# Optimization experiments

Hardware: AMD Instinct MI355X
Metric: run time of the kernel (lower is better)

The kernel has to match this reference:

```python
import jax, jax.numpy as jnp
import numpy as np

T, D, H, HD = 4096, 1536, 12, 128  # tokens, hidden, heads, head_dim
NEG = -1e9


def rotate_half(x):
    x1, x2 = jnp.split(x, 2, axis=-1)
    return jnp.concatenate((-x2, x1), axis=-1)


def setup_inputs() -> dict:
    key = jax.random.key(0)
    k1, k2, k3, k4 = jax.random.split(key, 4)
    hidden_states = jax.random.normal(k1, (T, D), dtype=jnp.float32)
    cu_seqlens = (jnp.arange(5, dtype=jnp.int32) * (T // 4))  # [0,1024,2048,3072,4096]
    # rotary angles: positions within each segment times inverse frequencies
    pos = jnp.arange(T, dtype=jnp.float32) % (T // 4)
    inv_freq = 1.0 / (10000.0 ** (jnp.arange(0, HD // 2, dtype=jnp.float32) / (HD // 2)))
    rotary_pos_emb = pos[:, None] * inv_freq[None, :]  # (T, HD//2)
    w_qkv = jax.random.normal(k2, (3 * D, D), dtype=jnp.float32) * (D ** -0.5)
    w_proj = jax.random.normal(k3, (D, D), dtype=jnp.float32) * (D ** -0.5)
    return {"hidden_states": hidden_states, "cu_seqlens": cu_seqlens,
            "rotary_pos_emb": rotary_pos_emb, "w_qkv": w_qkv, "w_proj": w_proj}


def reference(hidden_states, cu_seqlens, rotary_pos_emb, w_qkv, w_proj):
    seq_len = hidden_states.shape[0]
    scaling = HD ** -0.5
    # fused QKV projection: (T, 3D) -> (3, T, H, HD)
    qkv = (hidden_states @ w_qkv.T).reshape(seq_len, 3, H, HD).transpose(1, 0, 2, 3)
    q, k, v = qkv[0], qkv[1], qkv[2]
    # RoPE (vision style): emb = cat(rpe, rpe) along last dim
    emb = jnp.concatenate((rotary_pos_emb, rotary_pos_emb), axis=-1)  # (T, HD)
    cos = jnp.cos(emb)[:, None, :]  # (T, 1, HD) broadcast over heads
    sin = jnp.sin(emb)[:, None, :]
    q = q * cos + rotate_half(q) * sin
    k = k * cos + rotate_half(k) * sin
    # block-diagonal mask from cu_seqlens (varlen packing)
    seg_id = jnp.searchsorted(cu_seqlens[1:], jnp.arange(seq_len), side="right")
    block_mask = seg_id[:, None] == seg_id[None, :]  # (T, T) bool
    # attention per head: (H, T, HD)
    qh = q.transpose(1, 0, 2)
    kh = k.transpose(1, 0, 2)
    vh = v.transpose(1, 0, 2)
    scores = jnp.einsum("htd,hsd->hts", qh, kh) * scaling
    scores = jnp.where(block_mask[None, :, :], scores, NEG)
    attn = jax.nn.softmax(scores, axis=-1)
    out = jnp.einsum("hts,hsd->htd", attn, vh)  # (H, T, HD)
    out = out.transpose(1, 0, 2).reshape(seq_len, D)
    return out @ w_proj.T


if __name__ == "__main__":
    o = reference(**setup_inputs())
    print(o.shape, o.dtype)
```

## Files before the change

kernel.cpp:

```cpp
#include <hip/hip_runtime.h>
#include <stdint.h>

#define TT 4096
#define DD 1536
#define NH 12
#define HD_ 128

typedef __bf16 bf16x8 __attribute__((ext_vector_type(8)));
typedef float  f32x4  __attribute__((ext_vector_type(4)));
typedef float  f32x16 __attribute__((ext_vector_type(16)));

__device__ __forceinline__ unsigned short f2b(float f) {
  union { float f; uint32_t u; } x; x.f = f;
  uint32_t r = x.u + 0x7fffu + ((x.u >> 16) & 1u);
  return (unsigned short)(r >> 16);
}
__device__ __forceinline__ float b2f(unsigned short b) {
  union { uint32_t u; float f; } x; x.u = ((uint32_t)b) << 16;
  return x.f;
}

__device__ __forceinline__ f32x16 mfma32(bf16x8 a, bf16x8 b, f32x16 c) {
  return __builtin_amdgcn_mfma_f32_32x32x16_bf16(a, b, c, 0, 0, 0);
}

__device__ __forceinline__ void async16(const void* g, void* l) {
  __builtin_amdgcn_global_load_lds((const __attribute__((address_space(1))) uint32_t*)g,
                                   (__attribute__((address_space(3))) uint32_t*)l,
                                   16, 0, 0);
}

__global__ void aux_kernel(const float* __restrict__ hs,
                           const float* __restrict__ wqkv,
                           const float* __restrict__ rpe,
                           unsigned short* __restrict__ hb,
                           unsigned short* __restrict__ wq,
                           float* __restrict__ cs, float* __restrict__ sn) {
  const int b = blockIdx.x;
  if (b < 13056) {
    const float* in = (b < 6144) ? hs : wqkv;
    unsigned short* out = (b < 6144) ? hb : wq;
    const int base = (b < 6144) ? b : (b - 6144);
    int i = (base * 256 + threadIdx.x) * 4;
    float4 v = *reinterpret_cast<const float4*>(in + i);
    ushort4 o;
    o.x = f2b(v.x); o.y = f2b(v.y); o.z = f2b(v.z); o.w = f2b(v.w);
    *reinterpret_cast<ushort4*>(out + i) = o;
  } else {
    int i = (b - 13056) * 256 + threadIdx.x;
    float e = rpe[i];
    float s, c;
    sincosf(e, &s, &c);
    cs[i] = c;
    sn[i] = s;
  }
}

__global__ void cast_bf16_kernel(const float* __restrict__ in,
                                 unsigned short* __restrict__ out, int n) {
  int i = (blockIdx.x * blockDim.x + threadIdx.x) * 4;
  if (i + 3 < n) {
    float4 v = *reinterpret_cast<const float4*>(in + i);
    ushort4 o;
    o.x = f2b(v.x); o.y = f2b(v.y); o.z = f2b(v.z); o.w = f2b(v.w);
    *reinterpret_cast<ushort4*>(out + i) = o;
  }
}

__global__ __launch_bounds__(256, 4) void gemm_qkv_kernel(
    const unsigned short* __restrict__ A, const unsigned short* __restrict__ B,
    unsigned short* __restrict__ Qp, unsigned short* __restrict__ Kp,
    unsigned short* __restrict__ Vt, const float* __restrict__ csT,
    const float* __restrict__ snT) {
  __shared__ char smem[32768];
  const int tid = threadIdx.x;
  const int lane = tid & 63;
  const int wave = tid >> 6;
  const int wm = wave >> 1, wn = wave & 1;
  const int lr = lane & 15, lh = lane >> 4;

  const int m0 = blockIdx.x * 128;
  const int n0 = blockIdx.y * 128;

  const int srow = tid >> 2;
  const int schunk = (tid & 3) ^ (srow & 3);
  const unsigned short* Ag = A + (size_t)(m0 + srow) * DD + schunk * 8;
  const unsigned short* Bg = B + (size_t)(n0 + srow) * DD + schunk * 8;

#define STAGE_G(BUF, K0)                                            \
  {                                                                 \
    unsigned short* la = (unsigned short*)(smem + (BUF) * 16384);   \
    unsigned short* lb = la + 4096;                                 \
    async16(Ag + (K0), &la[tid * 8]);                               \
    async16(Ag + (K0) + (size_t)64 * DD, &la[2048 + tid * 8]);      \
    async16(Bg + (K0), &lb[tid * 8]);                               \
    async16(Bg + (K0) + (size_t)64 * DD, &lb[2048 + tid * 8]);      \
  }

  const int csw = (lr & 3);
  f32x4 acc[4][4] = {};
  STAGE_G(0, 0);
  __syncthreads();
  int cur = 0;
  for (int k0 = 0; k0 < DD; k0 += 32) {
    const int kn = (k0 + 32 < DD) ? (k0 + 32) : k0;
    STAGE_G(cur ^ 1, kn);
    const unsigned short* la = (const unsigned short*)(smem + cur * 16384);
    const unsigned short* lb = la + 4096;
    bf16x8 af[4], bfr[4];
#pragma unroll
    for (int i = 0; i < 4; i++) {
      af[i]  = *reinterpret_cast<const bf16x8*>(
          &la[(wm * 64 + i * 16 + lr) * 32 + (lh ^ csw) * 8]);
      bfr[i] = *reinterpret_cast<const bf16x8*>(
          &lb[(i * 32 + wn * 16 + lr) * 32 + (lh ^ csw) * 8]);
    }
#pragma unroll
    for (int i = 0; i < 4; i++)
#pragma unroll
      for (int j = 0; j < 4; j++)
        acc[i][j] = __builtin_amdgcn_mfma_f32_16x16x32_bf16(af[i], bfr[j], acc[i][j], 0, 0, 0);
    __syncthreads();
    cur ^= 1;
  }
#undef STAGE_G

  const int s  = n0 / DD;
  const int hh = (n0 - s * DD) >> 7;

  if (s == 2) {
#pragma unroll
    for (int i = 0; i < 4; i++)
#pragma unroll
      for (int j = 0; j < 4; j++) {
        const int dd = j * 32 + wn * 16 + lr;
        const int t0 = m0 + wm * 64 + i * 16 + lh * 4;
        ushort4 st;
        st.x = f2b(acc[i][j][0]); st.y = f2b(acc[i][j][1]);
        st.z = f2b(acc[i][j][2]); st.w = f2b(acc[i][j][3]);
        *reinterpret_cast<ushort4*>(&Vt[((size_t)(hh * HD_ + dd)) * TT + t0]) = st;
      }
  } else {
    unsigned short* dst = (s == 0) ? Qp : Kp;
    const float scale =
        (s == 0) ? (0.08838834764831845f * 1.4426950408889634f) : 1.0f;
#pragma unroll
    for (int i = 0; i < 4; i++) {
#pragma unroll
      for (int j = 0; j < 4; j++) {
        const int dd = j * 32 + wn * 16 + lr;
        const int d2 = dd & 63;
        const float sgn = (dd < 64) ? -1.f : 1.f;
#pragma unroll
        for (int r = 0; r < 4; r++) {
          const int t = m0 + wm * 64 + i * 16 + lh * 4 + r;
          const float own = acc[i][j][r];
          const float par = acc[i][j ^ 2][r];
          const float c   = csT[t * 64 + d2];
          const float sn_ = snT[t * 64 + d2];
          dst[((size_t)hh * TT + t) * HD_ + dd] =
              f2b((own * c + sgn * par * sn_) * scale);
        }
        __builtin_amdgcn_sched_barrier(0);
      }
    }
  }
}

__global__ __launch_bounds__(512) void attn_kernel(
    const unsigned short* __restrict__ Qp, const unsigned short* __restrict__ Kp,
    const unsigned short* __restrict__ Vt, const int* __restrict__ cu,
    unsigned short* __restrict__ AO) {
  __shared__ unsigned short lds[32768];
  const int bid = blockIdx.x;
  const int tid = threadIdx.x;
  const int wave = tid >> 6;
  const int lane = tid & 63;
  const int lq = lane & 31;
  const int hi = lane >> 5;
  const int swz = lq & 7;

  const int xcd  = bid & 7;
  const int idx  = bid >> 3;
  const int pair = xcd * 6 + (idx >> 2);
  const int qblk = idx & 3;
  const int h    = pair >> 2;
  const int seg  = pair & 3;
  const int kstart = cu[seg], kend = cu[seg + 1];
  const int q0 = kstart + (qblk * 8 + wave) * 32;

  const unsigned short* Kh = Kp + (size_t)h * TT * HD_;
  const unsigned short* Vh = Vt + (size_t)h * HD_ * TT;

  const int krow0 = tid >> 4, kc0 = tid & 15;
  const int vrow0 = tid >> 3, vc0 = tid & 7;

#define STAGE_TILE(BUF, KT)                                                    \
  {                                                                            \
    unsigned short* Lk = &lds[(BUF) * 16384];                                  \
    unsigned short* Lv = Lk + 8192;                                            \
    _Pragma("unroll")                                                          \
    for (int r = 0; r < 2; r++) {                                              \
      int row = krow0 + r * 32;                                                \
      int c = kc0 ^ (row & 7);                                                 \
      async16(Kh + (size_t)((KT) + row) * HD_ + c * 8, Lk + tid * 8 + r * 4096); \
    }                                                                          \
    _Pragma("unroll")                                                          \
    for (int r = 0; r < 2; r++) {                                              \
      int row = vrow0 + r * 64;                                                \
      int c = vc0 ^ (row & 7);                                                 \
      async16(Vh + (size_t)row * TT + (KT) + c * 8, Lv + tid * 8 + r * 4096);  \
    }                                                                          \
  }

  const unsigned short* Qg = Qp + ((size_t)h * TT + q0 + lq) * HD_ + hi * 8;
  bf16x8 qf[8];
#pragma unroll
  for (int s = 0; s < 8; s++)
    qf[s] = *reinterpret_cast<const bf16x8*>(Qg + s * 16);

  STAGE_TILE(0, kstart);
  __syncthreads();

  f32x16 o0 = {}, o1 = {}, o2 = {}, o3 = {};
  float lsum = 0.f;
  int cur = 0;

  for (int kt = kstart; kt < kend; kt += 64) {
    const int ktn = (kt + 64 < kend) ? (kt + 64) : kt;
    STAGE_TILE(cur ^ 1, ktn);

    const unsigned short* Kl = &lds[cur * 16384];
    const unsigned short* Vl = Kl + 8192;

    f32x16 sA = {}, sB = {};
#pragma unroll
    for (int s = 0; s < 8; s++) {
      bf16x8 kf = *reinterpret_cast<const bf16x8*>(
          Kl + lq * 128 + (((s << 1) | hi) ^ swz) * 8);
      sA = mfma32(kf, qf[s], sA);
    }
#pragma unroll
    for (int s = 0; s < 8; s++) {
      bf16x8 kf = *reinterpret_cast<const bf16x8*>(
          Kl + 4096 + lq * 128 + (((s << 1) | hi) ^ swz) * 8);
      sB = mfma32(kf, qf[s], sB);
    }

    bf16x8 pfrag[4];
    float acc0 = 0.f, acc1 = 0.f;
#pragma unroll
    for (int g = 0; g < 4; g++) {
      const f32x16 S = (g & 2) ? sB : sA;
      const int b = (g & 1) * 8;
      float e0 = __builtin_amdgcn_exp2f(S[b + 0]);
      float e1 = __builtin_amdgcn_exp2f(S[b + 1]);
      float e2 = __builtin_amdgcn_exp2f(S[b + 2]);
      float e3 = __builtin_amdgcn_exp2f(S[b + 3]);
      float e4 = __builtin_amdgcn_exp2f(S[b + 4]);
      float e5 = __builtin_amdgcn_exp2f(S[b + 5]);
      float e6 = __builtin_amdgcn_exp2f(S[b + 6]);
      float e7 = __builtin_amdgcn_exp2f(S[b + 7]);
      acc0 += (e0 + e1) + (e2 + e3);
      acc1 += (e4 + e5) + (e6 + e7);
      union PW { uint32_t u; __bf16 e[2]; } p0, p1, p2, p3;
      p0.e[0] = (__bf16)e0; p0.e[1] = (__bf16)e1;
      p1.e[0] = (__bf16)e2; p1.e[1] = (__bf16)e3;
      p2.e[0] = (__bf16)e4; p2.e[1] = (__bf16)e5;
      p3.e[0] = (__bf16)e6; p3.e[1] = (__bf16)e7;
      uint32_t W2 = (uint32_t)__shfl_xor((int)(hi ? p0.u : p2.u), 32);
      uint32_t W3 = (uint32_t)__shfl_xor((int)(hi ? p1.u : p3.u), 32);
      union F { uint32_t w[4]; bf16x8 v; } f;
      f.w[0] = hi ? W2 : p0.u;
      f.w[1] = hi ? W3 : p1.u;
      f.w[2] = hi ? p2.u : W2;
      f.w[3] = hi ? p3.u : W3;
      pfrag[g] = f.v;
    }
    float tsum = acc0 + acc1;
    lsum += tsum + __shfl_xor(tsum, 32);

#pragma unroll
    for (int g = 0; g < 4; g++) {
      const int co = (((g << 1) | hi) ^ swz) * 8;
      bf16x8 v0 = *reinterpret_cast<const bf16x8*>(Vl + (lq)       * 64 + co);
      bf16x8 v1 = *reinterpret_cast<const bf16x8*>(Vl + (32 + lq)  * 64 + co);
      bf16x8 v2 = *reinterpret_cast<const bf16x8*>(Vl + (64 + lq)  * 64 + co);
      bf16x8 v3 = *reinterpret_cast<const bf16x8*>(Vl + (96 + lq)  * 64 + co);
      o0 = mfma32(v0, pfrag[g], o0);
      o1 = mfma32(v1, pfrag[g], o1);
      o2 = mfma32(v2, pfrag[g], o2);
      o3 = mfma32(v3, pfrag[g], o3);
    }

    __syncthreads();
    cur ^= 1;
  }
#undef STAGE_TILE

  const float inv = 1.0f / lsum;
  unsigned short* Ab = AO + (size_t)(q0 + lq) * DD + h * HD_ + 4 * hi;
#pragma unroll
  for (int dblk = 0; dblk < 4; dblk++) {
    f32x16 o = (dblk == 0) ? o0 : (dblk == 1) ? o1 : (dblk == 2) ? o2 : o3;
#pragma unroll
    for (int rq = 0; rq < 4; rq++) {
      ushort4 st;
      st.x = f2b(o[rq * 4 + 0] * inv);
      st.y = f2b(o[rq * 4 + 1] * inv);
      st.z = f2b(o[rq * 4 + 2] * inv);
      st.w = f2b(o[rq * 4 + 3] * inv);
      *reinterpret_cast<ushort4*>(Ab + dblk * 32 + rq * 8) = st;
    }
  }
}

__global__ __launch_bounds__(256, 4) void gemm_out_kernel(
    const unsigned short* __restrict__ A, const unsigned short* __restrict__ B,
    float* __restrict__ C) {
  __shared__ char smem[32768];
  const int tid = threadIdx.x;
  const int lane = tid & 63;
  const int wave = tid >> 6;
  const int wm = wave >> 1, wn = wave & 1;
  const int lr = lane & 15, lh = lane >> 4;
  const int m0 = blockIdx.x * 128, n0 = blockIdx.y * 128;

  const int srow = tid >> 2;
  const int schunk = (tid & 3) ^ (srow & 3);
  const unsigned short* Ag = A + (size_t)(m0 + srow) * DD + schunk * 8;
  const unsigned short* Bg = B + (size_t)(n0 + srow) * DD + schunk * 8;

#define STAGE_G(BUF, K0)                                            \
  {                                                                 \
    unsigned short* la = (unsigned short*)(smem + (BUF) * 16384);   \
    unsigned short* lb = la + 4096;                                 \
    async16(Ag + (K0), &la[tid * 8]);                               \
    async16(Ag + (K0) + (size_t)64 * DD, &la[2048 + tid * 8]);      \
    async16(Bg + (K0), &lb[tid * 8]);                               \
    async16(Bg + (K0) + (size_t)64 * DD, &lb[2048 + tid * 8]);      \
  }

  const int csw = (lr & 3);
  f32x4 acc[4][4] = {};
  STAGE_G(0, 0);
  __syncthreads();
  int cur = 0;
  for (int k0 = 0; k0 < DD; k0 += 32) {
    const int kn = (k0 + 32 < DD) ? (k0 + 32) : k0;
    STAGE_G(cur ^ 1, kn);
    const unsigned short* la = (const unsigned short*)(smem + cur * 16384);
    const unsigned short* lb = la + 4096;
    bf16x8 af[4], bfr[4];
#pragma unroll
    for (int i = 0; i < 4; i++) {
      af[i]  = *reinterpret_cast<const bf16x8*>(
          &la[(wm * 64 + i * 16 + lr) * 32 + (lh ^ csw) * 8]);
      bfr[i] = *reinterpret_cast<const bf16x8*>(
          &lb[(wn * 64 + i * 16 + lr) * 32 + (lh ^ csw) * 8]);
    }
#pragma unroll
    for (int i = 0; i < 4; i++)
#pragma unroll
      for (int j = 0; j < 4; j++)
        acc[i][j] = __builtin_amdgcn_mfma_f32_16x16x32_bf16(af[i], bfr[j], acc[i][j], 0, 0, 0);
    __syncthreads();
    cur ^= 1;
  }
#undef STAGE_G

#pragma unroll
  for (int i = 0; i < 4; i++)
#pragma unroll
    for (int j = 0; j < 4; j++) {
      int cn = n0 + wn * 64 + j * 16 + lr;
#pragma unroll
      for (int r = 0; r < 4; r++) {
        int t = m0 + wm * 64 + i * 16 + lh * 4 + r;
        C[(size_t)t * DD + cn] = acc[i][j][r];
      }
    }
}

extern "C" void kernel_launch(void* const* d_in, const int* in_sizes, int n_in,
                              void* d_out, int out_size, void* d_ws, size_t ws_size,
                              hipStream_t stream) {
  const float* hs    = (const float*)d_in[0];
  const int*   cu    = (const int*)d_in[1];
  const float* rpe   = (const float*)d_in[2];
  const float* wqkv  = (const float*)d_in[3];
  const float* wproj = (const float*)d_in[4];
  float* out = (float*)d_out;
  char* ws = (char*)d_ws;

  unsigned short* hb = (unsigned short*)(ws + 0);
  unsigned short* wq = (unsigned short*)(ws + 12582912);
  unsigned short* wp = (unsigned short*)(ws + 26738688);
  unsigned short* Qp = (unsigned short*)(ws + 31457280);
  unsigned short* Kp = (unsigned short*)(ws + 44040192);
  unsigned short* Vt = (unsigned short*)(ws + 56623104);

  float* csT = (float*)wp;
  float* snT = csT + TT * 64;

  aux_kernel<<<14080, 256, 0, stream>>>(hs, wqkv, rpe, hb, wq, csT, snT);

  gemm_qkv_kernel<<<dim3(32, 36), 256, 0, stream>>>(hb, wq, Qp, Kp, Vt, csT, snT);

  cast_bf16_kernel<<<2304, 256, 0, stream>>>(wproj, wp, DD * DD);

  attn_kernel<<<192, 512, 0, stream>>>(Qp, Kp, Vt, cu, hb );

  gemm_out_kernel<<<dim3(32, 12), 256, 0, stream>>>(hb , wp, out);
}
```

Before: 169.0 us.

## Triple-buffer GEMM LDS staging and fold wproj cast into aux kernel

Both GEMM kernels move from double-buffered to triple-buffered LDS staging. They prefetch two k-tiles ahead and use a partial vmcnt wait plus a raw barrier instead of a full __syncthreads, to hide global load latency. The separate wproj bf16 cast kernel is merged into the aux kernel, dropping one launch. Because wp is now written early, the cos/sin tables move into the output buffer as scratch. The cost is 48KB of LDS per block, which may reduce occupancy, and the hand-tuned waitcnt adds correctness risk.

```diff
diff --git a/kernel.cpp b/kernel.cpp
--- a/kernel.cpp
+++ b/kernel.cpp
@@ -30,24 +30,35 @@
                                    16, 0, 0);
 }
 
+__device__ __forceinline__ void barrier_vm4() {
+  asm volatile("s_waitcnt vmcnt(4)" ::: "memory");
+  __builtin_amdgcn_s_barrier();
+  __builtin_amdgcn_sched_barrier(0);
+}
+
 __global__ void aux_kernel(const float* __restrict__ hs,
                            const float* __restrict__ wqkv,
+                           const float* __restrict__ wproj,
                            const float* __restrict__ rpe,
                            unsigned short* __restrict__ hb,
                            unsigned short* __restrict__ wq,
+                           unsigned short* __restrict__ wp,
                            float* __restrict__ cs, float* __restrict__ sn) {
   const int b = blockIdx.x;
-  if (b < 13056) {
-    const float* in = (b < 6144) ? hs : wqkv;
-    unsigned short* out = (b < 6144) ? hb : wq;
-    const int base = (b < 6144) ? b : (b - 6144);
+  if (b < 15360) {
+    const float* in;
+    unsigned short* out;
+    int base;
+    if (b < 6144)       { in = hs;    out = hb; base = b; }
+    else if (b < 13056) { in = wqkv;  out = wq; base = b - 6144; }
+    else                { in = wproj; out = wp; base = b - 13056; }
     int i = (base * 256 + threadIdx.x) * 4;
     float4 v = *reinterpret_cast<const float4*>(in + i);
     ushort4 o;
     o.x = f2b(v.x); o.y = f2b(v.y); o.z = f2b(v.z); o.w = f2b(v.w);
     *reinterpret_cast<ushort4*>(out + i) = o;
   } else {
-    int i = (b - 13056) * 256 + threadIdx.x;
+    int i = (b - 15360) * 256 + threadIdx.x;
     float e = rpe[i];
     float s, c;
     sincosf(e, &s, &c);
@@ -56,23 +67,12 @@
   }
 }
 
-__global__ void cast_bf16_kernel(const float* __restrict__ in,
-                                 unsigned short* __restrict__ out, int n) {
-  int i = (blockIdx.x * blockDim.x + threadIdx.x) * 4;
-  if (i + 3 < n) {
-    float4 v = *reinterpret_cast<const float4*>(in + i);
-    ushort4 o;
-    o.x = f2b(v.x); o.y = f2b(v.y); o.z = f2b(v.z); o.w = f2b(v.w);
-    *reinterpret_cast<ushort4*>(out + i) = o;
-  }
-}
-
 __global__ __launch_bounds__(256, 4) void gemm_qkv_kernel(
     const unsigned short* __restrict__ A, const unsigned short* __restrict__ B,
     unsigned short* __restrict__ Qp, unsigned short* __restrict__ Kp,
     unsigned short* __restrict__ Vt, const float* __restrict__ csT,
     const float* __restrict__ snT) {
-  __shared__ char smem[32768];
+  __shared__ char smem[49152];
   const int tid = threadIdx.x;
   const int lane = tid & 63;
   const int wave = tid >> 6;
@@ -100,11 +100,13 @@
   const int csw = (lr & 3);
   f32x4 acc[4][4] = {};
   STAGE_G(0, 0);
-  __syncthreads();
+  STAGE_G(1, 32);
+  barrier_vm4();
   int cur = 0;
-  for (int k0 = 0; k0 < DD; k0 += 32) {
-    const int kn = (k0 + 32 < DD) ? (k0 + 32) : k0;
-    STAGE_G(cur ^ 1, kn);
+  for (int t = 0; t < 48; ++t) {
+    int k2 = (t + 2 < 48) ? (t + 2) : 47;
+    int nb = cur + 2; if (nb >= 3) nb -= 3;
+    STAGE_G(nb, k2 * 32);
     const unsigned short* la = (const unsigned short*)(smem + cur * 16384);
     const unsigned short* lb = la + 4096;
     bf16x8 af[4], bfr[4];
@@ -120,10 +122,11 @@
 #pragma unroll
       for (int j = 0; j < 4; j++)
         acc[i][j] = __builtin_amdgcn_mfma_f32_16x16x32_bf16(af[i], bfr[j], acc[i][j], 0, 0, 0);
-    __syncthreads();
-    cur ^= 1;
+    barrier_vm4();
+    cur = (cur == 2) ? 0 : cur + 1;
   }
 #undef STAGE_G
+  __builtin_amdgcn_sched_barrier(0);
 
   const int s  = n0 / DD;
   const int hh = (n0 - s * DD) >> 7;
@@ -318,7 +321,7 @@
 __global__ __launch_bounds__(256, 4) void gemm_out_kernel(
     const unsigned short* __restrict__ A, const unsigned short* __restrict__ B,
     float* __restrict__ C) {
-  __shared__ char smem[32768];
+  __shared__ char smem[49152];
   const int tid = threadIdx.x;
   const int lane = tid & 63;
   const int wave = tid >> 6;
@@ -344,11 +347,13 @@
   const int csw = (lr & 3);
   f32x4 acc[4][4] = {};
   STAGE_G(0, 0);
-  __syncthreads();
+  STAGE_G(1, 32);
+  barrier_vm4();
   int cur = 0;
-  for (int k0 = 0; k0 < DD; k0 += 32) {
-    const int kn = (k0 + 32 < DD) ? (k0 + 32) : k0;
-    STAGE_G(cur ^ 1, kn);
+  for (int t = 0; t < 48; ++t) {
+    int k2 = (t + 2 < 48) ? (t + 2) : 47;
+    int nb = cur + 2; if (nb >= 3) nb -= 3;
+    STAGE_G(nb, k2 * 32);
     const unsigned short* la = (const unsigned short*)(smem + cur * 16384);
     const unsigned short* lb = la + 4096;
     bf16x8 af[4], bfr[4];
@@ -364,10 +369,11 @@
 #pragma unroll
       for (int j = 0; j < 4; j++)
         acc[i][j] = __builtin_amdgcn_mfma_f32_16x16x32_bf16(af[i], bfr[j], acc[i][j], 0, 0, 0);
-    __syncthreads();
-    cur ^= 1;
+    barrier_vm4();
+    cur = (cur == 2) ? 0 : cur + 1;
   }
 #undef STAGE_G
+  __builtin_amdgcn_sched_barrier(0);
 
 #pragma unroll
   for (int i = 0; i < 4; i++)
@@ -400,15 +406,13 @@
   unsigned short* Kp = (unsigned short*)(ws + 44040192);
   unsigned short* Vt = (unsigned short*)(ws + 56623104);
 
-  float* csT = (float*)wp;
+  float* csT = out;
   float* snT = csT + TT * 64;
 
-  aux_kernel<<<14080, 256, 0, stream>>>(hs, wqkv, rpe, hb, wq, csT, snT);
+  aux_kernel<<<16384, 256, 0, stream>>>(hs, wqkv, wproj, rpe, hb, wq, wp, csT, snT);
 
   gemm_qkv_kernel<<<dim3(32, 36), 256, 0, stream>>>(hb, wq, Qp, Kp, Vt, csT, snT);
 
-  cast_bf16_kernel<<<2304, 256, 0, stream>>>(wproj, wp, DD * DD);
-
   attn_kernel<<<192, 512, 0, stream>>>(Qp, Kp, Vt, cu, hb );
 
   gemm_out_kernel<<<dim3(32, 12), 256, 0, stream>>>(hb , wp, out);
```

Measured after the change: 181.6 us. 7.5% more time.
